# Kernel optimization log

Hardware: AMD Instinct MI355X
Metric: run time of the kernel (lower is better)

The kernel has to match this reference:

```python
import jax, jax.numpy as jnp
import numpy as np

N, E = 50000, 1600000
IN, HID, HEADS, OUT = 128, 32, 4, 32
NEG_SLOPE = 0.2  # PyG GATConv default leaky_relu slope


def _glorot(k, shape):
    fan = shape[0] + shape[-1]
    return jax.random.normal(k, shape, dtype=jnp.float32) * np.sqrt(2.0 / fan).astype(np.float32)


def setup_inputs() -> dict:
    key = jax.random.key(0)
    ks = jax.random.split(key, 16)
    x = jax.random.normal(ks[0], (N, IN), dtype=jnp.float32)
    edge_index = jax.random.randint(ks[1], (2, E), 0, N, dtype=jnp.int32)
    # layer 0: in -> heads*hid, concat
    W0 = _glorot(ks[2], (IN, HEADS * HID))
    as0 = _glorot(ks[3], (HEADS, HID)); ad0 = _glorot(ks[4], (HEADS, HID))
    b0 = jnp.zeros((HEADS * HID,), jnp.float32)
    # layer 1: heads*hid -> heads*hid, concat
    W1 = _glorot(ks[5], (HEADS * HID, HEADS * HID))
    as1 = _glorot(ks[6], (HEADS, HID)); ad1 = _glorot(ks[7], (HEADS, HID))
    b1 = jnp.zeros((HEADS * HID,), jnp.float32)
    # layer 2: heads*hid -> out, heads=1, concat=False
    W2 = _glorot(ks[8], (HEADS * HID, OUT))
    as2 = _glorot(ks[9], (1, OUT)); ad2 = _glorot(ks[10], (1, OUT))
    b2 = jnp.zeros((OUT,), jnp.float32)
    return dict(x=x, edge_index=edge_index, W0=W0, as0=as0, ad0=ad0, b0=b0,
                W1=W1, as1=as1, ad1=ad1, b1=b1, W2=W2, as2=as2, ad2=ad2, b2=b2)


def gat_layer(x, src, dst, W, a_src, a_dst, b, heads, out_ch, concat):
    # linear transform per head: [N, heads, out_ch]
    h = (x @ W).reshape(N, heads, out_ch)
    # per-node attention half-logits: [N, heads]
    alpha_src = jnp.einsum('nhc,hc->nh', h, a_src)
    alpha_dst = jnp.einsum('nhc,hc->nh', h, a_dst)
    # per-edge logits (edge j -> i): [E', heads]
    logits = jax.nn.leaky_relu(alpha_src[src] + alpha_dst[dst], NEG_SLOPE)
    # segment softmax over incoming edges of each destination node
    m = jax.ops.segment_max(logits, dst, num_segments=N)
    e = jnp.exp(logits - m[dst])
    denom = jax.ops.segment_sum(e, dst, num_segments=N)
    alpha = e / denom[dst]
    # weighted message scatter-add: [N, heads, out_ch]
    out = jax.ops.segment_sum(h[src] * alpha[:, :, None], dst, num_segments=N)
    out = out.reshape(N, heads * out_ch) if concat else out.mean(axis=1)
    return out + b, alpha


def reference(x, edge_index, W0, as0, ad0, b0, W1, as1, ad1, b1, W2, as2, ad2, b2):
    # add self loops (PyG add_self_loops=True)
    loops = jnp.arange(N, dtype=edge_index.dtype)
    src = jnp.concatenate([edge_index[0], loops])
    dst = jnp.concatenate([edge_index[1], loops])

    h, alpha0 = gat_layer(x, src, dst, W0, as0, ad0, b0, HEADS, HID, True)
    h = jax.nn.elu(h)  # dropout inactive in eval mode
    h, _ = gat_layer(h, src, dst, W1, as1, ad1, b1, HEADS, HID, True)
    h = jax.nn.elu(h)
    out, _ = gat_layer(h, src, dst, W2, as2, ad2, b2, 1, OUT, False)
    return alpha0, out
```

## Files before the change

kernel.cpp:

```cpp
#include <hip/hip_runtime.h>
#include <math.h>

#define NN 50000
#define NEG 0.2f
#define TILE 4096

typedef __attribute__((ext_vector_type(8))) short short8;
typedef __attribute__((ext_vector_type(4))) float f32x4;

__device__ __forceinline__ unsigned short f2bf(float f){
    unsigned u = __float_as_uint(f);
    u += 0x7fffu + ((u >> 16) & 1u);
    return (unsigned short)(u >> 16);
}
__device__ __forceinline__ float bf2f(unsigned short v){
    return __uint_as_float(((unsigned)v) << 16);
}

__device__ __forceinline__ int excl_scan_256(int v, int* buf, int tid){
    buf[tid] = v;
    __syncthreads();
#pragma unroll
    for (int off = 1; off < 256; off <<= 1){
        int t = (tid >= off) ? buf[tid - off] : 0;
        __syncthreads();
        buf[tid] += t;
        __syncthreads();
    }
    return buf[tid] - v;
}

__global__ void k_zero(int* p, int n){
    int i = blockIdx.x * 256 + threadIdx.x;
    if (i < n) p[i] = 0;
}

__global__ __launch_bounds__(256) void k_binning(const int* __restrict__ ei, int E,
        int* __restrict__ bucketCount, unsigned* __restrict__ tmp){
    __shared__ unsigned stage[TILE];
    __shared__ int hist[256], sbuf[256], exs[256], cur[256], gbase[256];
    int tid = threadIdx.x;
    int EP = E + NN;
    int tileBase = blockIdx.x * TILE;
    int cnt = min(TILE, EP - tileBase);

    hist[tid] = 0;
    __syncthreads();

    unsigned packed[16];
#pragma unroll
    for (int k = 0; k < 16; ++k){
        int e = tileBase + tid + (k << 8);
        unsigned p = 0xffffffffu;
        if (e < EP){
            int s, d;
            if (e < E){ s = ei[e]; d = ei[E + e]; } else { s = e - E; d = s; }
            p = ((unsigned)d << 16) | (unsigned)s;
            atomicAdd(&hist[d >> 8], 1);
        }
        packed[k] = p;
    }
    __syncthreads();
    int h = hist[tid];
    int ex = excl_scan_256(h, sbuf, tid);
    exs[tid] = ex;
    cur[tid] = ex;
    __syncthreads();
#pragma unroll
    for (int k = 0; k < 16; ++k){
        unsigned p = packed[k];
        if (p != 0xffffffffu){
            int b = p >> 24;
            int pos = atomicAdd(&cur[b], 1);
            stage[pos] = p;
        }
    }
    gbase[tid] = atomicAdd(&bucketCount[tid], h);
    __syncthreads();
    for (int i = tid; i < cnt; i += 256){
        unsigned p = stage[i];
        int b = p >> 24;
        tmp[(b << 14) + gbase[b] + (i - exs[b])] = p;
    }
}

__global__ __launch_bounds__(256) void k_bucket_csr(int EP,
        const int* __restrict__ bucketCount, const unsigned* __restrict__ tmp,
        int* __restrict__ row_ptr, unsigned short* __restrict__ ssrc){
    __shared__ int sbuf[256], deg[256], cur[256];
    __shared__ int baseSh, nSh;
    int b = blockIdx.x;
    int tid = threadIdx.x;
    int c = bucketCount[tid];
    int exb = excl_scan_256(c, sbuf, tid);
    if (tid == b){ baseSh = exb; nSh = c; }
    deg[tid] = 0;
    __syncthreads();
    int base = baseSh, n = nSh;
    const unsigned* tb = tmp + ((size_t)b << 14);
    for (int i = tid; i < n; i += 256)
        atomicAdd(&deg[(tb[i] >> 16) & 255], 1);
    __syncthreads();
    int d = deg[tid];
    int dx = excl_scan_256(d, sbuf, tid);
    cur[tid] = dx;
    int dst = (b << 8) + tid;
    if (dst < NN) row_ptr[dst] = base + dx;
    if (b == 0 && tid == 0) row_ptr[NN] = EP;
    __syncthreads();
    for (int i = tid; i < n; i += 256){
        unsigned p = tb[i];
        int pos = atomicAdd(&cur[(p >> 16) & 255], 1);
        ssrc[base + pos] = (unsigned short)(p & 0xffffu);
    }
}

__global__ void k_packW(const float* __restrict__ W0, const float* __restrict__ W1,
                        const float* __restrict__ W2,
                        unsigned short* __restrict__ h0, unsigned short* __restrict__ l0,
                        unsigned short* __restrict__ h1, unsigned short* __restrict__ l1,
                        unsigned short* __restrict__ h2, unsigned short* __restrict__ l2){
    int t = blockIdx.x * 256 + threadIdx.x;
    const float* W; unsigned short *ph, *pl; int Ncol; int u;
    if (t < 16384){ W = W0; ph = h0; pl = l0; Ncol = 128; u = t; }
    else if (t < 32768){ W = W1; ph = h1; pl = l1; Ncol = 128; u = t - 16384; }
    else if (t < 36864){ W = W2; ph = h2; pl = l2; Ncol = 32;  u = t - 32768; }
    else return;
    int n = u >> 7, k = u & 127;
    float f = W[k * Ncol + n];
    unsigned short hi = f2bf(f);
    unsigned short lo = f2bf(f - bf2f(hi));
    ph[n * 128 + k] = hi;
    pl[n * 128 + k] = lo;
}

template<int NT>
__global__ __launch_bounds__(256) void k_gemm_mfma(
        const float* __restrict__ A,
        const unsigned short* __restrict__ Bhi,
        const unsigned short* __restrict__ Blo,
        float* __restrict__ C, unsigned short* __restrict__ Cbf, int M){
    const int Ncol = NT * 16;
    int wave = threadIdx.x >> 6;
    int lane = threadIdx.x & 63;
    int r    = lane & 15;
    int oct  = lane >> 4;
    int rowBase = blockIdx.x * 64 + wave * 16;

    f32x4 acc[NT];
#pragma unroll
    for (int c = 0; c < NT; ++c) acc[c] = (f32x4){0.f, 0.f, 0.f, 0.f};

    int lrow = rowBase + r; if (lrow > M - 1) lrow = M - 1;
    const float* arow = A + (size_t)lrow * 128;

    for (int t = 0; t < 4; ++t){
        int k0 = t * 32 + oct * 8;
        float4 a0 = *(const float4*)&arow[k0];
        float4 a1 = *(const float4*)&arow[k0 + 4];
        float av[8] = {a0.x, a0.y, a0.z, a0.w, a1.x, a1.y, a1.z, a1.w};
        short8 ahi, alo;
#pragma unroll
        for (int j = 0; j < 8; ++j){
            unsigned short h = f2bf(av[j]);
            unsigned short l = f2bf(av[j] - bf2f(h));
            ahi[j] = (short)h; alo[j] = (short)l;
        }
#pragma unroll
        for (int c = 0; c < NT; ++c){
            short8 bhi = *(const short8*)&Bhi[(c * 16 + r) * 128 + k0];
            short8 blo = *(const short8*)&Blo[(c * 16 + r) * 128 + k0];
            acc[c] = __builtin_amdgcn_mfma_f32_16x16x32_bf16(ahi, bhi, acc[c], 0, 0, 0);
            acc[c] = __builtin_amdgcn_mfma_f32_16x16x32_bf16(alo, bhi, acc[c], 0, 0, 0);
            acc[c] = __builtin_amdgcn_mfma_f32_16x16x32_bf16(ahi, blo, acc[c], 0, 0, 0);
        }
    }
#pragma unroll
    for (int c = 0; c < NT; ++c){
#pragma unroll
        for (int reg = 0; reg < 4; ++reg){
            int row = rowBase + oct * 4 + reg;
            if (row < M){
                int col = c * 16 + r;
                float v = acc[c][reg];
                C[(size_t)row * Ncol + col] = v;
                if (Cbf) Cbf[(size_t)row * Ncol + col] = f2bf(v);
            }
        }
    }
}

__global__ void k_nodealpha(const float* __restrict__ h,
                            const float* __restrict__ a_s,
                            const float* __restrict__ a_d,
                            float* __restrict__ asrc, float* __restrict__ adst,
                            int H, int C){
    int t = blockIdx.x * 256 + threadIdx.x;
    if (t >= NN * H) return;
    int n = t / H, hd = t % H;
    const float* hp = h + (size_t)n * H * C + hd * C;
    float s1 = 0.f, s2 = 0.f;
    for (int c = 0; c < C; c += 4){
        float4 hv = *(const float4*)&hp[c];
        float4 av = *(const float4*)&a_s[hd * C + c];
        float4 dv = *(const float4*)&a_d[hd * C + c];
        s1 += hv.x * av.x + hv.y * av.y + hv.z * av.z + hv.w * av.w;
        s2 += hv.x * dv.x + hv.y * dv.y + hv.z * dv.z + hv.w * dv.w;
    }
    asrc[t] = s1;
    adst[t] = s2;
}

__global__ __launch_bounds__(256) void k_agg4m(
        const uint4* __restrict__ hb4,
        const float* __restrict__ asrc, const float* __restrict__ adst,
        const int* __restrict__ row_ptr, const unsigned short* __restrict__ ssrc,
        const float* __restrict__ bias, float* __restrict__ outp,
        float* __restrict__ gm, float* __restrict__ gdenom, int writeStats){
    int wave = (blockIdx.x * 256 + threadIdx.x) >> 6;
    int lane = threadIdx.x & 63;
    if (wave >= NN) return;
    int i = wave;
    int lo = row_ptr[i], hi = row_ptr[i + 1];

    int hd = lane & 3;
    int s  = lane >> 2;
    float adv1 = adst[i * 4 + hd];
    float m = -3.0e38f, sum = 0.f;
    for (int idx = lo + s; idx < hi; idx += 16){
        unsigned j = ssrc[idx];
        float lg = asrc[j * 4u + hd] + adv1;
        lg = fmaxf(lg, NEG * lg);
        float nm = fmaxf(m, lg);
        sum = sum * __expf(m - nm) + __expf(lg - nm);
        m = nm;
    }
    for (int off = 4; off < 64; off <<= 1){
        float mo = __shfl_xor(m, off);
        float so = __shfl_xor(sum, off);
        float nm = fmaxf(m, mo);
        float pa = (m  == nm) ? sum : sum * __expf(m - nm);
        float pb = (mo == nm) ? so  : so  * __expf(mo - nm);
        m = nm; sum = pa + pb;
    }
    if (writeStats && s == 0){
        gm[i * 4 + hd] = m;
        gdenom[i * 4 + hd] = sum;
    }

    int g = lane >> 4;
    int q = lane & 15;
    int myh = q >> 2;
    float mh = __shfl(m, myh);
    float rs = 1.f / __shfl(sum, myh);
    float adv = adst[i * 4 + myh];

    float acc[8];
#pragma unroll
    for (int k = 0; k < 8; ++k) acc[k] = 0.f;

    int idx = lo;
#define AGG4_BODY(JJ) {                                                       \
        float lg = asrc[(JJ) * 4u + myh] + adv;                               \
        lg = fmaxf(lg, NEG * lg);                                             \
        float a = __expf(lg - mh) * rs;                                       \
        uint4 gv = hb4[(JJ) * 16u + (unsigned)q];                             \
        acc[0] += a * __uint_as_float(gv.x << 16);                            \
        acc[1] += a * __uint_as_float(gv.x & 0xffff0000u);                    \
        acc[2] += a * __uint_as_float(gv.y << 16);                            \
        acc[3] += a * __uint_as_float(gv.y & 0xffff0000u);                    \
        acc[4] += a * __uint_as_float(gv.z << 16);                            \
        acc[5] += a * __uint_as_float(gv.z & 0xffff0000u);                    \
        acc[6] += a * __uint_as_float(gv.w << 16);                            \
        acc[7] += a * __uint_as_float(gv.w & 0xffff0000u); }
    for (; idx + 4 <= hi; idx += 4){
        unsigned j = ssrc[idx + g];
        AGG4_BODY(j)
    }
    if (idx + g < hi){
        unsigned j = ssrc[idx + g];
        AGG4_BODY(j)
    }
#undef AGG4_BODY
#pragma unroll
    for (int k = 0; k < 8; ++k){
        acc[k] += __shfl_xor(acc[k], 16);
        acc[k] += __shfl_xor(acc[k], 32);
    }
    if (g == 0){
        int c0 = q * 8;
        float4 bA = *(const float4*)&bias[c0];
        float4 bB = *(const float4*)&bias[c0 + 4];
        float o[8] = {acc[0] + bA.x, acc[1] + bA.y, acc[2] + bA.z, acc[3] + bA.w,
                      acc[4] + bB.x, acc[5] + bB.y, acc[6] + bB.z, acc[7] + bB.w};
#pragma unroll
        for (int k = 0; k < 8; ++k)
            o[k] = (o[k] > 0.f) ? o[k] : (__expf(o[k]) - 1.f);
        *(float4*)&outp[(size_t)i * 128 + c0]     = make_float4(o[0], o[1], o[2], o[3]);
        *(float4*)&outp[(size_t)i * 128 + c0 + 4] = make_float4(o[4], o[5], o[6], o[7]);
    }
}

__global__ void k_alpha0(const int* __restrict__ ei, int E,
                         const float4* __restrict__ asrc4, const float4* __restrict__ adst4,
                         const float4* __restrict__ gm4, const float4* __restrict__ gd4,
                         float4* __restrict__ out){
    int e = blockIdx.x * 256 + threadIdx.x;
    int EP = E + NN;
    if (e >= EP) return;
    int s, d;
    if (e < E){ s = ei[e]; d = ei[E + e]; } else { s = e - E; d = s; }
    float4 as = asrc4[s], ad = adst4[d], mm = gm4[d], dn = gd4[d];
    float4 r;
    float lg;
    lg = as.x + ad.x; lg = fmaxf(lg, NEG * lg); r.x = __expf(lg - mm.x) / dn.x;
    lg = as.y + ad.y; lg = fmaxf(lg, NEG * lg); r.y = __expf(lg - mm.y) / dn.y;
    lg = as.z + ad.z; lg = fmaxf(lg, NEG * lg); r.z = __expf(lg - mm.z) / dn.z;
    lg = as.w + ad.w; lg = fmaxf(lg, NEG * lg); r.w = __expf(lg - mm.w) / dn.w;
    out[e] = r;
}

__global__ __launch_bounds__(256) void k_agg1m(
        const float4* __restrict__ h24,
        const float* __restrict__ asrc, const float* __restrict__ adst,
        const int* __restrict__ row_ptr, const unsigned short* __restrict__ ssrc,
        const float* __restrict__ bias, float* __restrict__ outp){
    int wave = (blockIdx.x * 256 + threadIdx.x) >> 6;
    int lane = threadIdx.x & 63;
    if (wave >= NN) return;
    int i = wave;
    int lo = row_ptr[i], hi = row_ptr[i + 1];

    float adv = adst[i];
    float m = -3.0e38f, sum = 0.f;
    for (int idx = lo + lane; idx < hi; idx += 64){
        unsigned j = ssrc[idx];
        float lg = asrc[j] + adv;
        lg = fmaxf(lg, NEG * lg);
        float nm = fmaxf(m, lg);
        sum = sum * __expf(m - nm) + __expf(lg - nm);
        m = nm;
    }
    for (int off = 1; off < 64; off <<= 1){
        float mo = __shfl_xor(m, off);
        float so = __shfl_xor(sum, off);
        float nm = fmaxf(m, mo);
        float pa = (m  == nm) ? sum : sum * __expf(m - nm);
        float pb = (mo == nm) ? so  : so  * __expf(mo - nm);
        m = nm; sum = pa + pb;
    }
    float rs = 1.f / sum;

    int g = lane >> 3;
    int q = lane & 7;
    float acc[4] = {0.f, 0.f, 0.f, 0.f};
    int idx = lo;
    for (; idx + 8 <= hi; idx += 8){
        unsigned j = ssrc[idx + g];
        float lg = asrc[j] + adv;
        lg = fmaxf(lg, NEG * lg);
        float a = __expf(lg - m) * rs;
        float4 v = h24[(unsigned)j * 8u + (unsigned)q];
        acc[0] += a * v.x; acc[1] += a * v.y;
        acc[2] += a * v.z; acc[3] += a * v.w;
    }
    if (idx + g < hi){
        unsigned j = ssrc[idx + g];
        float lg = asrc[j] + adv;
        lg = fmaxf(lg, NEG * lg);
        float a = __expf(lg - m) * rs;
        float4 v = h24[(unsigned)j * 8u + (unsigned)q];
        acc[0] += a * v.x; acc[1] += a * v.y;
        acc[2] += a * v.z; acc[3] += a * v.w;
    }
#pragma unroll
    for (int k = 0; k < 4; ++k){
        acc[k] += __shfl_xor(acc[k], 8);
        acc[k] += __shfl_xor(acc[k], 16);
        acc[k] += __shfl_xor(acc[k], 32);
    }
    if (g == 0){
        float4 b = *(const float4*)&bias[q * 4];
        *(float4*)&outp[(size_t)i * 32 + q * 4] =
            make_float4(acc[0] + b.x, acc[1] + b.y, acc[2] + b.z, acc[3] + b.w);
    }
}

extern "C" void kernel_launch(void* const* d_in, const int* in_sizes, int n_in,
                              void* d_out, int out_size, void* d_ws, size_t ws_size,
                              hipStream_t stream){
    const float* x   = (const float*)d_in[0];
    const int*   ei  = (const int*)  d_in[1];
    const float* W0  = (const float*)d_in[2];
    const float* as0 = (const float*)d_in[3];
    const float* ad0 = (const float*)d_in[4];
    const float* b0  = (const float*)d_in[5];
    const float* W1  = (const float*)d_in[6];
    const float* as1 = (const float*)d_in[7];
    const float* ad1 = (const float*)d_in[8];
    const float* b1  = (const float*)d_in[9];
    const float* W2  = (const float*)d_in[10];
    const float* as2 = (const float*)d_in[11];
    const float* ad2 = (const float*)d_in[12];
    const float* b2  = (const float*)d_in[13];

    const int E  = in_sizes[1] / 2;
    const int EP = E + NN;

    char* w = (char*)d_ws;
    size_t off = 0;
    auto carve = [&](size_t bytes) -> char* {
        char* p = w + off;
        off += (bytes + 255) & ~(size_t)255;
        return p;
    };
    int*            bucketCount = (int*)       carve(sizeof(int) * 256);
    int*            row_ptr = (int*)           carve(sizeof(int) * (NN + 1));
    unsigned short* ssrc    = (unsigned short*)carve(sizeof(short) * (size_t)EP);
    float*          hbuf    = (float*)         carve(sizeof(float) * (size_t)NN * 128);
    unsigned short* hb16    = (unsigned short*)carve(sizeof(short) * (size_t)NN * 128);
    float*          post    = (float*)         carve(sizeof(float) * (size_t)NN * 128);
    float*          asrc    = (float*)         carve(sizeof(float) * NN * 4);
    float*          adst    = (float*)         carve(sizeof(float) * NN * 4);
    float*          gm      = (float*)         carve(sizeof(float) * NN * 4);
    float*          gdenom  = (float*)         carve(sizeof(float) * NN * 4);
    unsigned short* Whi0    = (unsigned short*)carve(sizeof(short) * 16384);
    unsigned short* Wlo0    = (unsigned short*)carve(sizeof(short) * 16384);
    unsigned short* Whi1    = (unsigned short*)carve(sizeof(short) * 16384);
    unsigned short* Wlo1    = (unsigned short*)carve(sizeof(short) * 16384);
    unsigned short* Whi2    = (unsigned short*)carve(sizeof(short) * 4096);
    unsigned short* Wlo2    = (unsigned short*)carve(sizeof(short) * 4096);
    unsigned*       tmp     = (unsigned*)post;

    float* out_alpha = (float*)d_out;
    float* out_final = (float*)d_out + (size_t)EP * 4;

    const int edgeBlocks = (EP + 255) / 256;
    const int waveBlocks = (NN + 3) / 4;
    const int gemmBlocks = (NN + 63) / 64;

    k_zero      <<<1, 256, 0, stream>>>(bucketCount, 256);
    k_binning   <<<(EP + TILE - 1) / TILE, 256, 0, stream>>>(ei, E, bucketCount, tmp);
    k_bucket_csr<<<256, 256, 0, stream>>>(EP, bucketCount, tmp, row_ptr, ssrc);
    k_packW     <<<144, 256, 0, stream>>>(W0, W1, W2, Whi0, Wlo0, Whi1, Wlo1, Whi2, Wlo2);

    k_gemm_mfma<8><<<gemmBlocks, 256, 0, stream>>>(x, Whi0, Wlo0, hbuf, hb16, NN);
    k_nodealpha<<<(NN * 4 + 255) / 256, 256, 0, stream>>>(hbuf, as0, ad0, asrc, adst, 4, 32);
    k_agg4m<<<waveBlocks, 256, 0, stream>>>((const uint4*)hb16, asrc, adst, row_ptr,
                                            ssrc, b0, post, gm, gdenom, 1);
    k_alpha0<<<edgeBlocks, 256, 0, stream>>>(ei, E, (const float4*)asrc, (const float4*)adst,
                                             (const float4*)gm, (const float4*)gdenom,
                                             (float4*)out_alpha);

    k_gemm_mfma<8><<<gemmBlocks, 256, 0, stream>>>(post, Whi1, Wlo1, hbuf, hb16, NN);
    k_nodealpha<<<(NN * 4 + 255) / 256, 256, 0, stream>>>(hbuf, as1, ad1, asrc, adst, 4, 32);
    k_agg4m<<<waveBlocks, 256, 0, stream>>>((const uint4*)hb16, asrc, adst, row_ptr,
                                            ssrc, b1, post, gm, gdenom, 0);

    k_gemm_mfma<2><<<gemmBlocks, 256, 0, stream>>>(post, Whi2, Wlo2, hbuf, nullptr, NN);
    k_nodealpha<<<(NN + 255) / 256, 256, 0, stream>>>(hbuf, as2, ad2, asrc, adst, 1, 32);
    k_agg1m<<<waveBlocks, 256, 0, stream>>>((const float4*)hbuf, asrc, adst, row_ptr,
                                            ssrc, b2, out_final);
}
```

Measured before the change: 481.4 us.

## Drop max-subtraction pass; compute softmax denominator during single aggregation pass

Removes the separate online max/sum pass over each node's incoming edges in the aggregation kernels. Unnormalized exp(logit) weights are accumulated together with the denominator, and the result is normalized at the end. This halves the gather traffic on asrc/ssrc and drops the gm buffer and its reads in the alpha kernel. The risk is numerical: without max subtraction, exp could overflow for large logits, which relies on the logits staying small for these inputs.

```diff
diff --git a/kernel.cpp b/kernel.cpp
--- a/kernel.cpp
+++ b/kernel.cpp
@@ -211,59 +211,33 @@
     adst[t] = s2;
 }
 
-__global__ __launch_bounds__(256) void k_agg4m(
+__global__ __launch_bounds__(256) void k_agg4s(
         const uint4* __restrict__ hb4,
         const float* __restrict__ asrc, const float* __restrict__ adst,
         const int* __restrict__ row_ptr, const unsigned short* __restrict__ ssrc,
         const float* __restrict__ bias, float* __restrict__ outp,
-        float* __restrict__ gm, float* __restrict__ gdenom, int writeStats){
+        float* __restrict__ gdenom, int writeStats){
     int wave = (blockIdx.x * 256 + threadIdx.x) >> 6;
     int lane = threadIdx.x & 63;
     if (wave >= NN) return;
     int i = wave;
     int lo = row_ptr[i], hi = row_ptr[i + 1];
-
-    int hd = lane & 3;
-    int s  = lane >> 2;
-    float adv1 = adst[i * 4 + hd];
-    float m = -3.0e38f, sum = 0.f;
-    for (int idx = lo + s; idx < hi; idx += 16){
-        unsigned j = ssrc[idx];
-        float lg = asrc[j * 4u + hd] + adv1;
-        lg = fmaxf(lg, NEG * lg);
-        float nm = fmaxf(m, lg);
-        sum = sum * __expf(m - nm) + __expf(lg - nm);
-        m = nm;
-    }
-    for (int off = 4; off < 64; off <<= 1){
-        float mo = __shfl_xor(m, off);
-        float so = __shfl_xor(sum, off);
-        float nm = fmaxf(m, mo);
-        float pa = (m  == nm) ? sum : sum * __expf(m - nm);
-        float pb = (mo == nm) ? so  : so  * __expf(mo - nm);
-        m = nm; sum = pa + pb;
-    }
-    if (writeStats && s == 0){
-        gm[i * 4 + hd] = m;
-        gdenom[i * 4 + hd] = sum;
-    }
-
     int g = lane >> 4;
     int q = lane & 15;
     int myh = q >> 2;
-    float mh = __shfl(m, myh);
-    float rs = 1.f / __shfl(sum, myh);
     float adv = adst[i * 4 + myh];
 
     float acc[8];
 #pragma unroll
     for (int k = 0; k < 8; ++k) acc[k] = 0.f;
+    float dsum = 0.f;
 
     int idx = lo;
 #define AGG4_BODY(JJ) {                                                       \
         float lg = asrc[(JJ) * 4u + myh] + adv;                               \
         lg = fmaxf(lg, NEG * lg);                                             \
-        float a = __expf(lg - mh) * rs;                                       \
+        float a = __expf(lg);                                                 \
+        dsum += a;                                                            \
         uint4 gv = hb4[(JJ) * 16u + (unsigned)q];                             \
         acc[0] += a * __uint_as_float(gv.x << 16);                            \
         acc[1] += a * __uint_as_float(gv.x & 0xffff0000u);                    \
@@ -287,12 +261,21 @@
         acc[k] += __shfl_xor(acc[k], 16);
         acc[k] += __shfl_xor(acc[k], 32);
     }
+    dsum += __shfl_xor(dsum, 16);
+    dsum += __shfl_xor(dsum, 32);
+
+    if (writeStats && g == 0 && (q & 3) == 0)
+        gdenom[i * 4 + myh] = dsum;
+
     if (g == 0){
+        float rs = 1.f / dsum;
         int c0 = q * 8;
         float4 bA = *(const float4*)&bias[c0];
         float4 bB = *(const float4*)&bias[c0 + 4];
-        float o[8] = {acc[0] + bA.x, acc[1] + bA.y, acc[2] + bA.z, acc[3] + bA.w,
-                      acc[4] + bB.x, acc[5] + bB.y, acc[6] + bB.z, acc[7] + bB.w};
+        float o[8] = {acc[0] * rs + bA.x, acc[1] * rs + bA.y,
+                      acc[2] * rs + bA.z, acc[3] * rs + bA.w,
+                      acc[4] * rs + bB.x, acc[5] * rs + bB.y,
+                      acc[6] * rs + bB.z, acc[7] * rs + bB.w};
 #pragma unroll
         for (int k = 0; k < 8; ++k)
             o[k] = (o[k] > 0.f) ? o[k] : (__expf(o[k]) - 1.f);
@@ -303,24 +286,23 @@
 
 __global__ void k_alpha0(const int* __restrict__ ei, int E,
                          const float4* __restrict__ asrc4, const float4* __restrict__ adst4,
-                         const float4* __restrict__ gm4, const float4* __restrict__ gd4,
-                         float4* __restrict__ out){
+                         const float4* __restrict__ gd4, float4* __restrict__ out){
     int e = blockIdx.x * 256 + threadIdx.x;
     int EP = E + NN;
     if (e >= EP) return;
     int s, d;
     if (e < E){ s = ei[e]; d = ei[E + e]; } else { s = e - E; d = s; }
-    float4 as = asrc4[s], ad = adst4[d], mm = gm4[d], dn = gd4[d];
+    float4 as = asrc4[s], ad = adst4[d], dn = gd4[d];
     float4 r;
     float lg;
-    lg = as.x + ad.x; lg = fmaxf(lg, NEG * lg); r.x = __expf(lg - mm.x) / dn.x;
-    lg = as.y + ad.y; lg = fmaxf(lg, NEG * lg); r.y = __expf(lg - mm.y) / dn.y;
-    lg = as.z + ad.z; lg = fmaxf(lg, NEG * lg); r.z = __expf(lg - mm.z) / dn.z;
-    lg = as.w + ad.w; lg = fmaxf(lg, NEG * lg); r.w = __expf(lg - mm.w) / dn.w;
+    lg = as.x + ad.x; lg = fmaxf(lg, NEG * lg); r.x = __expf(lg) / dn.x;
+    lg = as.y + ad.y; lg = fmaxf(lg, NEG * lg); r.y = __expf(lg) / dn.y;
+    lg = as.z + ad.z; lg = fmaxf(lg, NEG * lg); r.z = __expf(lg) / dn.z;
+    lg = as.w + ad.w; lg = fmaxf(lg, NEG * lg); r.w = __expf(lg) / dn.w;
     out[e] = r;
 }
 
-__global__ __launch_bounds__(256) void k_agg1m(
+__global__ __launch_bounds__(256) void k_agg1s(
         const float4* __restrict__ h24,
         const float* __restrict__ asrc, const float* __restrict__ adst,
         const int* __restrict__ row_ptr, const unsigned short* __restrict__ ssrc,
@@ -330,36 +312,19 @@
     if (wave >= NN) return;
     int i = wave;
     int lo = row_ptr[i], hi = row_ptr[i + 1];
-
-    float adv = adst[i];
-    float m = -3.0e38f, sum = 0.f;
-    for (int idx = lo + lane; idx < hi; idx += 64){
-        unsigned j = ssrc[idx];
-        float lg = asrc[j] + adv;
-        lg = fmaxf(lg, NEG * lg);
-        float nm = fmaxf(m, lg);
-        sum = sum * __expf(m - nm) + __expf(lg - nm);
-        m = nm;
-    }
-    for (int off = 1; off < 64; off <<= 1){
-        float mo = __shfl_xor(m, off);
-        float so = __shfl_xor(sum, off);
-        float nm = fmaxf(m, mo);
-        float pa = (m  == nm) ? sum : sum * __expf(m - nm);
-        float pb = (mo == nm) ? so  : so  * __expf(mo - nm);
-        m = nm; sum = pa + pb;
-    }
-    float rs = 1.f / sum;
-
     int g = lane >> 3;
     int q = lane & 7;
+    float adv = adst[i];
+
     float acc[4] = {0.f, 0.f, 0.f, 0.f};
+    float dsum = 0.f;
     int idx = lo;
     for (; idx + 8 <= hi; idx += 8){
         unsigned j = ssrc[idx + g];
         float lg = asrc[j] + adv;
         lg = fmaxf(lg, NEG * lg);
-        float a = __expf(lg - m) * rs;
+        float a = __expf(lg);
+        dsum += a;
         float4 v = h24[(unsigned)j * 8u + (unsigned)q];
         acc[0] += a * v.x; acc[1] += a * v.y;
         acc[2] += a * v.z; acc[3] += a * v.w;
@@ -368,7 +333,8 @@
         unsigned j = ssrc[idx + g];
         float lg = asrc[j] + adv;
         lg = fmaxf(lg, NEG * lg);
-        float a = __expf(lg - m) * rs;
+        float a = __expf(lg);
+        dsum += a;
         float4 v = h24[(unsigned)j * 8u + (unsigned)q];
         acc[0] += a * v.x; acc[1] += a * v.y;
         acc[2] += a * v.z; acc[3] += a * v.w;
@@ -379,10 +345,15 @@
         acc[k] += __shfl_xor(acc[k], 16);
         acc[k] += __shfl_xor(acc[k], 32);
     }
+    dsum += __shfl_xor(dsum, 8);
+    dsum += __shfl_xor(dsum, 16);
+    dsum += __shfl_xor(dsum, 32);
     if (g == 0){
+        float rs = 1.f / dsum;
         float4 b = *(const float4*)&bias[q * 4];
         *(float4*)&outp[(size_t)i * 32 + q * 4] =
-            make_float4(acc[0] + b.x, acc[1] + b.y, acc[2] + b.z, acc[3] + b.w);
+            make_float4(acc[0] * rs + b.x, acc[1] * rs + b.y,
+                        acc[2] * rs + b.z, acc[3] * rs + b.w);
     }
 }
 
@@ -422,7 +393,6 @@
     float*          post    = (float*)         carve(sizeof(float) * (size_t)NN * 128);
     float*          asrc    = (float*)         carve(sizeof(float) * NN * 4);
     float*          adst    = (float*)         carve(sizeof(float) * NN * 4);
-    float*          gm      = (float*)         carve(sizeof(float) * NN * 4);
     float*          gdenom  = (float*)         carve(sizeof(float) * NN * 4);
     unsigned short* Whi0    = (unsigned short*)carve(sizeof(short) * 16384);
     unsigned short* Wlo0    = (unsigned short*)carve(sizeof(short) * 16384);
@@ -446,19 +416,18 @@
 
     k_gemm_mfma<8><<<gemmBlocks, 256, 0, stream>>>(x, Whi0, Wlo0, hbuf, hb16, NN);
     k_nodealpha<<<(NN * 4 + 255) / 256, 256, 0, stream>>>(hbuf, as0, ad0, asrc, adst, 4, 32);
-    k_agg4m<<<waveBlocks, 256, 0, stream>>>((const uint4*)hb16, asrc, adst, row_ptr,
-                                            ssrc, b0, post, gm, gdenom, 1);
+    k_agg4s<<<waveBlocks, 256, 0, stream>>>((const uint4*)hb16, asrc, adst, row_ptr,
+                                            ssrc, b0, post, gdenom, 1);
     k_alpha0<<<edgeBlocks, 256, 0, stream>>>(ei, E, (const float4*)asrc, (const float4*)adst,
-                                             (const float4*)gm, (const float4*)gdenom,
-                                             (float4*)out_alpha);
+                                             (const float4*)gdenom, (float4*)out_alpha);
 
     k_gemm_mfma<8><<<gemmBlocks, 256, 0, stream>>>(post, Whi1, Wlo1, hbuf, hb16, NN);
     k_nodealpha<<<(NN * 4 + 255) / 256, 256, 0, stream>>>(hbuf, as1, ad1, asrc, adst, 4, 32);
-    k_agg4m<<<waveBlocks, 256, 0, stream>>>((const uint4*)hb16, asrc, adst, row_ptr,
-                                            ssrc, b1, post, gm, gdenom, 0);
+    k_agg4s<<<waveBlocks, 256, 0, stream>>>((const uint4*)hb16, asrc, adst, row_ptr,
+                                            ssrc, b1, post, gdenom, 0);
 
     k_gemm_mfma<2><<<gemmBlocks, 256, 0, stream>>>(post, Whi2, Wlo2, hbuf, nullptr, NN);
     k_nodealpha<<<(NN + 255) / 256, 256, 0, stream>>>(hbuf, as2, ad2, asrc, adst, 1, 32);
-    k_agg1m<<<waveBlocks, 256, 0, stream>>>((const float4*)hbuf, asrc, adst, row_ptr,
+    k_agg1s<<<waveBlocks, 256, 0, stream>>>((const float4*)hbuf, asrc, adst, row_ptr,
                                             ssrc, b2, out_final);
 }
```

After: 444.6 us. 7.6% less time.
